# Kernel tuning notes

Hardware: AMD Instinct MI355X
Metric: run time of the kernel (lower is better)

## Reference

```python
import jax, jax.numpy as jnp
import numpy as np

# Hard-coded module constants (from source)
E = 384      # EMBEDDING_SIZE
H = 6        # HEAD_NO
HS = 64      # HEAD_SIZE = E // H
T_CTX = 256  # CONTEXT_LENGTH
L = 6        # LAYER_NO
V = 50257    # vocab_size (init kwarg)
B = 16       # batch
T = 256      # sequence length (== context length)


def setup_inputs() -> dict:
    key = jax.random.key(0)
    ks = jax.random.split(key, 12)
    p = lambda k, shape: jax.random.normal(k, shape, dtype=jnp.float32) * 0.02
    return {
        "idx": jax.random.randint(ks[0], (B, T), 0, V),
        "tok_emb": p(ks[1], (V, E)),
        "pos_emb": p(ks[2], (T_CTX, E)),
        # per-layer stacked params; per-head q/k/v weights concatenated into [E, E]
        "Wq": p(ks[3], (L, E, E)),
        "Wk": p(ks[4], (L, E, E)),
        "Wv": p(ks[5], (L, E, E)),
        "Wo": p(ks[6], (L, E, E)),
        "bo": jnp.zeros((L, E), jnp.float32),
        "ln1_g": jnp.ones((L, E), jnp.float32),
        "ln1_b": jnp.zeros((L, E), jnp.float32),
        "ln2_g": jnp.ones((L, E), jnp.float32),
        "ln2_b": jnp.zeros((L, E), jnp.float32),
        "Wm": p(ks[7], (L, E, E)),  # MLP: single Linear(E,E) + ReLU
        "bm": jnp.zeros((L, E), jnp.float32),
        "lnf_g": jnp.ones((E,), jnp.float32),
        "lnf_b": jnp.zeros((E,), jnp.float32),
        "Wlm": p(ks[8], (E, V)),
        "blm": jnp.zeros((V,), jnp.float32),
    }


def _layernorm(x, g, b):
    mu = jnp.mean(x, axis=-1, keepdims=True)
    var = jnp.var(x, axis=-1, keepdims=True)  # biased, matches torch LayerNorm
    return (x - mu) / jnp.sqrt(var + 1e-5) * g + b


def _forward(idx, tok_emb, pos_emb, Wq, Wk, Wv, Wo, bo, ln1_g, ln1_b,
             ln2_g, ln2_b, Wm, bm, lnf_g, lnf_b, Wlm, blm):
    Bb, Tt = idx.shape
    x = tok_emb[idx] + pos_emb[:Tt]                        # [B,T,E]
    causal = jnp.tril(jnp.ones((Tt, Tt), bool))            # tril buffer
    scale = 1.0 / jnp.sqrt(jnp.float32(HS))

    def block(x, lp):
        wq, wk, wv, wo, bo_, g1, b1, g2, b2, wm, bm_ = lp
        h = _layernorm(x, g1, b1)
        q = (h @ wq).reshape(Bb, Tt, H, HS)
        k = (h @ wk).reshape(Bb, Tt, H, HS)
        v = (h @ wv).reshape(Bb, Tt, H, HS)
        s = jnp.einsum('bqhd,bkhd->bhqk', q, k)
        # source: masked_fill(-inf) then divide by sqrt(HS); -inf stays -inf
        s = jnp.where(causal, s, -jnp.inf) * scale
        a = jax.nn.softmax(s, axis=-1)                     # dropout: eval mode (no-op)
        o = jnp.einsum('bhqk,bkhd->bqhd', a, v).reshape(Bb, Tt, E)
        x = x + (o @ wo + bo_)                             # proj + residual
        h2 = _layernorm(x, g2, b2)
        x = x + jax.nn.relu(h2 @ wm + bm_)                 # MLP is Linear+ReLU only
        return x, None

    x, _ = jax.lax.scan(block, x, (Wq, Wk, Wv, Wo, bo, ln1_g, ln1_b,
                                   ln2_g, ln2_b, Wm, bm))
    x = _layernorm(x, lnf_g, lnf_b)
    return x @ Wlm + blm                                   # [B,T,V] logits


def reference(idx, tok_emb, pos_emb, Wq, Wk, Wv, Wo, bo, ln1_g, ln1_b,
              ln2_g, ln2_b, Wm, bm, lnf_g, lnf_b, Wlm, blm):
    return _forward(idx, tok_emb, pos_emb, Wq, Wk, Wv, Wo, bo, ln1_g, ln1_b,
                    ln2_g, ln2_b, Wm, bm, lnf_g, lnf_b, Wlm, blm)
```

## Files before the change

kernel.cpp:

```cpp
#include <hip/hip_runtime.h>
#include <hip/hip_bf16.h>
#include <math.h>

#define E_DIM 384
#define N_HEAD 6
#define HEAD_SZ 64
#define SEQ 256
#define BATCH 16
#define NTOK 4096
#define NLAYER 6
#define VOCAB 50257
#define VPAD 50304
#define QKV_N 1152
#define NBH 96

typedef __attribute__((ext_vector_type(8))) short bf16x8;
typedef __attribute__((ext_vector_type(4))) float f32x4;

__device__ __forceinline__ void gload16(const void* g, void* l) {
    __builtin_amdgcn_global_load_lds((const __attribute__((address_space(1))) char*)g,
                                     (__attribute__((address_space(3))) char*)l, 16, 0, 0);
}

__global__ void embed_kernel(const int* __restrict__ idx,
                             const float* __restrict__ tok,
                             const float* __restrict__ pos,
                             float* __restrict__ x) {
    int i = blockIdx.x * blockDim.x + threadIdx.x;
    if (i >= NTOK * E_DIM) return;
    int m = i / E_DIM, e = i - m * E_DIM;
    int t = m & (SEQ - 1);
    x[i] = tok[(size_t)idx[m] * E_DIM + e] + pos[t * E_DIM + e];
}

__global__ __launch_bounds__(256) void ln_kernel(const float* __restrict__ x,
                                                 const float* __restrict__ g,
                                                 const float* __restrict__ b,
                                                 __hip_bfloat16* __restrict__ h) {
    int lane = threadIdx.x & 63;
    int wave = threadIdx.x >> 6;
    int row  = blockIdx.x * 4 + wave;
    const float* xr = x + (size_t)row * E_DIM;
    float v[6];
    float s = 0.f;
#pragma unroll
    for (int c = 0; c < 6; ++c) { v[c] = xr[lane + 64 * c]; s += v[c]; }
#pragma unroll
    for (int off = 32; off > 0; off >>= 1) s += __shfl_xor(s, off);
    float mu = s * (1.0f / E_DIM);
    float s2 = 0.f;
#pragma unroll
    for (int c = 0; c < 6; ++c) { float d = v[c] - mu; s2 += d * d; }
#pragma unroll
    for (int off = 32; off > 0; off >>= 1) s2 += __shfl_xor(s2, off);
    float rstd = rsqrtf(s2 * (1.0f / E_DIM) + 1e-5f);
    __hip_bfloat16* hr = h + (size_t)row * E_DIM;
#pragma unroll
    for (int c = 0; c < 6; ++c) {
        int e = lane + 64 * c;
        hr[e] = __float2bfloat16((v[c] - mu) * rstd * g[e] + b[e]);
    }
}

__device__ __forceinline__ void tconv_tile(const float* __restrict__ src,
                                           __hip_bfloat16* __restrict__ dst,
                                           int K, int N, int n0, int k0) {
    __shared__ float tbuf[64][65];
    int c = threadIdx.x & 63, r4 = threadIdx.x >> 6;
#pragma unroll
    for (int i = 0; i < 16; ++i) {
        int r = r4 * 16 + i;
        float v = 0.f;
        if (n0 + c < N) v = src[(size_t)(k0 + r) * N + n0 + c];
        tbuf[r][c] = v;
    }
    __syncthreads();
#pragma unroll
    for (int i = 0; i < 16; ++i) {
        int rn = r4 * 16 + i;
        dst[(size_t)(n0 + rn) * K + k0 + c] = __float2bfloat16(tbuf[c][rn]);
    }
}

__global__ __launch_bounds__(256) void tconv_layers(const float* __restrict__ Wq,
                                                    const float* __restrict__ Wk,
                                                    const float* __restrict__ Wv,
                                                    const float* __restrict__ Wo,
                                                    const float* __restrict__ Wm,
                                                    __hip_bfloat16* __restrict__ WtL) {
    int z = blockIdx.z;
    int l = z / 5, t = z - l * 5;
    const float* src;
    int dstoff;
    switch (t) {
        case 0: src = Wq; dstoff = 0;    break;
        case 1: src = Wk; dstoff = 384;  break;
        case 2: src = Wv; dstoff = 768;  break;
        case 3: src = Wo; dstoff = 1152; break;
        default: src = Wm; dstoff = 1536;
    }
    src += (size_t)l * E_DIM * E_DIM;
    __hip_bfloat16* dst = WtL + ((size_t)l * 1920 + dstoff) * E_DIM;
    tconv_tile(src, dst, E_DIM, E_DIM, blockIdx.x * 64, blockIdx.y * 64);
}

__global__ __launch_bounds__(256) void tconv_lm(const float* __restrict__ Wlm,
                                                __hip_bfloat16* __restrict__ dst) {
    tconv_tile(Wlm, dst, E_DIM, VOCAB, blockIdx.x * 64, blockIdx.y * 64);
}

__global__ __launch_bounds__(256) void qkvgemm(const __hip_bfloat16* __restrict__ A,
                                               const __hip_bfloat16* __restrict__ Bt,
                                               __hip_bfloat16* __restrict__ qb,
                                               __hip_bfloat16* __restrict__ kb,
                                               __hip_bfloat16* __restrict__ vt) {
    __shared__ __align__(1024) char lds[32768];
    char* Ar = lds;
    char* Br = lds + 16384;
    int tid = threadIdx.x;
    int lane = tid & 63, w = tid >> 6;
    int wm = w >> 1, wn = w & 1;
    int row0 = blockIdx.y * 128;
    int col0 = blockIdx.x * 128;

    f32x4 acc[4][4];
#pragma unroll
    for (int i = 0; i < 4; ++i)
#pragma unroll
        for (int j = 0; j < 4; ++j) acc[i][j] = (f32x4){0.f, 0.f, 0.f, 0.f};

    for (int k0 = 0; k0 < E_DIM; k0 += 64) {
        __syncthreads();
#pragma unroll
        for (int i = 0; i < 4; ++i) {
            int p  = i * 4096 + tid * 16;
            int lg = p ^ (((p >> 7) & 7) << 4);
            int r  = lg >> 7, cb = lg & 127;
            gload16((const char*)(A  + (size_t)(row0 + r) * E_DIM + k0) + cb, Ar + i * 4096 + w * 1024);
            gload16((const char*)(Bt + (size_t)(col0 + r) * E_DIM + k0) + cb, Br + i * 4096 + w * 1024);
        }
        __syncthreads();
#pragma unroll
        for (int ks = 0; ks < 2; ++ks) {
            bf16x8 af[4], bfr[4];
#pragma unroll
            for (int mi = 0; mi < 4; ++mi) {
                int rl = wm * 64 + mi * 16 + (lane & 15);
                int lg = rl * 128 + ks * 64 + ((lane >> 4) << 4);
                int ph = lg ^ ((rl & 7) << 4);
                af[mi] = *(const bf16x8*)(Ar + ph);
            }
#pragma unroll
            for (int ni = 0; ni < 4; ++ni) {
                int rl = wn * 64 + ni * 16 + (lane & 15);
                int lg = rl * 128 + ks * 64 + ((lane >> 4) << 4);
                int ph = lg ^ ((rl & 7) << 4);
                bfr[ni] = *(const bf16x8*)(Br + ph);
            }
#pragma unroll
            for (int mi = 0; mi < 4; ++mi)
#pragma unroll
                for (int ni = 0; ni < 4; ++ni)
                    acc[mi][ni] = __builtin_amdgcn_mfma_f32_16x16x32_bf16(
                        af[mi], bfr[ni], acc[mi][ni], 0, 0, 0);
        }
    }

#pragma unroll
    for (int mi = 0; mi < 4; ++mi) {
#pragma unroll
        for (int ni = 0; ni < 4; ++ni) {
            int gcl = col0 + wn * 64 + ni * 16 + (lane & 15);
            int which = gcl / 384;
            int rem = gcl - which * 384;
            int h = rem >> 6, d = rem & 63;
            int gr0 = row0 + wm * 64 + mi * 16 + ((lane >> 4) << 2);
#pragma unroll
            for (int j = 0; j < 4; ++j) {
                int gr = gr0 + j;
                int b = gr >> 8, t = gr & 255;
                int bh = b * N_HEAD + h;
                __hip_bfloat16 v = __float2bfloat16(acc[mi][ni][j]);
                if (which == 0)      qb[(((size_t)bh << 8) + t) * 64 + d] = v;
                else if (which == 1) kb[(((size_t)bh << 8) + t) * 64 + d] = v;
                else                 vt[(((size_t)bh << 6) + d) * SEQ + t] = v;
            }
        }
    }
}

template <int RELU>
__global__ __launch_bounds__(256) void egemm_ln(const __hip_bfloat16* __restrict__ A,
                                                const __hip_bfloat16* __restrict__ Bt,
                                                const float* __restrict__ bias,
                                                const float* __restrict__ xin,
                                                float* __restrict__ xout,
                                                const float* __restrict__ g,
                                                const float* __restrict__ bvec,
                                                __hip_bfloat16* __restrict__ hout) {
    __shared__ __align__(1024) char lds[53248];
    char* Breg = lds;
    char* Areg = lds + 49152;
    float* xt = (float*)lds;
    int tid = threadIdx.x;
    int lane = tid & 63, w = tid >> 6;
    int row0 = blockIdx.x * 32;

    f32x4 acc[2][6];
#pragma unroll
    for (int i = 0; i < 2; ++i)
#pragma unroll
        for (int j = 0; j < 6; ++j) acc[i][j] = (f32x4){0.f, 0.f, 0.f, 0.f};

    for (int k0 = 0; k0 < E_DIM; k0 += 64) {
        __syncthreads();
        {
            int p  = tid * 16;
            int lg = p ^ (((p >> 7) & 7) << 4);
            int r  = lg >> 7, cb = lg & 127;
            gload16((const char*)(A + (size_t)(row0 + r) * E_DIM + k0) + cb, Areg + w * 1024);
        }
#pragma unroll
        for (int i = 0; i < 12; ++i) {
            int p  = i * 4096 + tid * 16;
            int lg = p ^ (((p >> 7) & 7) << 4);
            int r  = lg >> 7, cb = lg & 127;
            gload16((const char*)(Bt + (size_t)r * E_DIM + k0) + cb, Breg + i * 4096 + w * 1024);
        }
        __syncthreads();
#pragma unroll
        for (int ks = 0; ks < 2; ++ks) {
            bf16x8 af[2], bfr[6];
#pragma unroll
            for (int mi = 0; mi < 2; ++mi) {
                int rl = mi * 16 + (lane & 15);
                int lg = rl * 128 + ks * 64 + ((lane >> 4) << 4);
                int ph = lg ^ ((rl & 7) << 4);
                af[mi] = *(const bf16x8*)(Areg + ph);
            }
#pragma unroll
            for (int ni = 0; ni < 6; ++ni) {
                int rl = w * 96 + ni * 16 + (lane & 15);
                int lg = rl * 128 + ks * 64 + ((lane >> 4) << 4);
                int ph = lg ^ ((rl & 7) << 4);
                bfr[ni] = *(const bf16x8*)(Breg + ph);
            }
#pragma unroll
            for (int mi = 0; mi < 2; ++mi)
#pragma unroll
                for (int ni = 0; ni < 6; ++ni)
                    acc[mi][ni] = __builtin_amdgcn_mfma_f32_16x16x32_bf16(
                        af[mi], bfr[ni], acc[mi][ni], 0, 0, 0);
        }
    }
    __syncthreads();

#pragma unroll
    for (int mi = 0; mi < 2; ++mi) {
#pragma unroll
        for (int ni = 0; ni < 6; ++ni) {
            int gc = w * 96 + ni * 16 + (lane & 15);
            int lr0 = mi * 16 + ((lane >> 4) << 2);
            float bv = bias[gc];
#pragma unroll
            for (int j = 0; j < 4; ++j) {
                int lr = lr0 + j;
                float u = acc[mi][ni][j] + bv;
                if (RELU) u = fmaxf(u, 0.f);
                float xn = xin[(size_t)(row0 + lr) * E_DIM + gc] + u;
                xout[(size_t)(row0 + lr) * E_DIM + gc] = xn;
                xt[lr * 392 + gc] = xn;
            }
        }
    }
    __syncthreads();

#pragma unroll
    for (int r8 = 0; r8 < 8; ++r8) {
        int r = w * 8 + r8;
        float v[6];
        float s = 0.f;
#pragma unroll
        for (int c = 0; c < 6; ++c) { v[c] = xt[r * 392 + lane + 64 * c]; s += v[c]; }
#pragma unroll
        for (int off = 32; off > 0; off >>= 1) s += __shfl_xor(s, off);
        float mu = s * (1.0f / E_DIM);
        float s2 = 0.f;
#pragma unroll
        for (int c = 0; c < 6; ++c) { float d = v[c] - mu; s2 += d * d; }
#pragma unroll
        for (int off = 32; off > 0; off >>= 1) s2 += __shfl_xor(s2, off);
        float rstd = rsqrtf(s2 * (1.0f / E_DIM) + 1e-5f);
        __hip_bfloat16* hr = hout + (size_t)(row0 + r) * E_DIM;
#pragma unroll
        for (int c = 0; c < 6; ++c) {
            int e = lane + 64 * c;
            hr[e] = __float2bfloat16((v[c] - mu) * rstd * g[e] + bvec[e]);
        }
    }
}

__global__ __launch_bounds__(256) void mgemm_lm(const __hip_bfloat16* __restrict__ A,
                                                const __hip_bfloat16* __restrict__ Bt,
                                                const float* __restrict__ bias,
                                                float* __restrict__ C) {
    __shared__ __align__(1024) char lds[32768];
    char* Ar = lds;
    char* Br = lds + 16384;
    int tid = threadIdx.x;
    int lane = tid & 63, w = tid >> 6;
    int wm = w >> 1, wn = w & 1;
    int row0 = blockIdx.y * 128;
    int col0 = blockIdx.x * 128;

    f32x4 acc[4][4];
#pragma unroll
    for (int i = 0; i < 4; ++i)
#pragma unroll
        for (int j = 0; j < 4; ++j) acc[i][j] = (f32x4){0.f, 0.f, 0.f, 0.f};

    for (int k0 = 0; k0 < E_DIM; k0 += 64) {
        __syncthreads();
#pragma unroll
        for (int i = 0; i < 4; ++i) {
            int p  = i * 4096 + tid * 16;
            int lg = p ^ (((p >> 7) & 7) << 4);
            int r  = lg >> 7, cb = lg & 127;
            gload16((const char*)(A  + (size_t)(row0 + r) * E_DIM + k0) + cb, Ar + i * 4096 + w * 1024);
            gload16((const char*)(Bt + (size_t)(col0 + r) * E_DIM + k0) + cb, Br + i * 4096 + w * 1024);
        }
        __syncthreads();
#pragma unroll
        for (int ks = 0; ks < 2; ++ks) {
            bf16x8 af[4], bfr[4];
#pragma unroll
            for (int mi = 0; mi < 4; ++mi) {
                int rl = wm * 64 + mi * 16 + (lane & 15);
                int lg = rl * 128 + ks * 64 + ((lane >> 4) << 4);
                int ph = lg ^ ((rl & 7) << 4);
                af[mi] = *(const bf16x8*)(Ar + ph);
            }
#pragma unroll
            for (int ni = 0; ni < 4; ++ni) {
                int rl = wn * 64 + ni * 16 + (lane & 15);
                int lg = rl * 128 + ks * 64 + ((lane >> 4) << 4);
                int ph = lg ^ ((rl & 7) << 4);
                bfr[ni] = *(const bf16x8*)(Br + ph);
            }
#pragma unroll
            for (int mi = 0; mi < 4; ++mi)
#pragma unroll
                for (int ni = 0; ni < 4; ++ni)
                    acc[mi][ni] = __builtin_amdgcn_mfma_f32_16x16x32_bf16(
                        af[mi], bfr[ni], acc[mi][ni], 0, 0, 0);
        }
    }

#pragma unroll
    for (int mi = 0; mi < 4; ++mi) {
#pragma unroll
        for (int ni = 0; ni < 4; ++ni) {
            int gr = row0 + wm * 64 + mi * 16 + ((lane >> 4) << 2);
            int gc = col0 + wn * 64 + ni * 16 + (lane & 15);
            if (gc < VOCAB) {
                float bv = bias[gc];
#pragma unroll
                for (int j = 0; j < 4; ++j)
                    C[(size_t)(gr + j) * VOCAB + gc] = acc[mi][ni][j] + bv;
            }
        }
    }
}

#define ATT_K 0
#define ATT_V 32768
#define ATT_Q 65536

__global__ __launch_bounds__(256) void attn_fused(const __hip_bfloat16* __restrict__ qb,
                                                  const __hip_bfloat16* __restrict__ kb,
                                                  const __hip_bfloat16* __restrict__ vt,
                                                  __hip_bfloat16* __restrict__ o) {
    __shared__ __align__(1024) char lds[73728];
    int tid = threadIdx.x;
    int lane = tid & 63, w = tid >> 6;
    int bh = blockIdx.x;
    int mq = blockIdx.y;
    int b = bh / N_HEAD, h = bh - b * N_HEAD;

    const char* kg = (const char*)(kb + (size_t)bh * SEQ * 64);
#pragma unroll
    for (int i = 0; i < 8; ++i) {
        int p = i * 4096 + tid * 16;
        int lg = p ^ (((p >> 7) & 7) << 4);
        gload16(kg + lg, lds + ATT_K + p);
    }
    const char* vg = (const char*)(vt + (size_t)bh * 64 * SEQ);
#pragma unroll
    for (int i = 0; i < 8; ++i) {
        int p = i * 4096 + tid * 16;
        int lg = p ^ (((p >> 9) & 7) << 4);
        gload16(vg + lg, lds + ATT_V + p);
    }
    const char* qg = (const char*)(qb + ((size_t)bh * SEQ + mq * 64) * 64);
#pragma unroll
    for (int i = 0; i < 2; ++i) {
        int p = i * 4096 + tid * 16;
        int lg = p ^ (((p >> 7) & 7) << 4);
        gload16(qg + lg, lds + ATT_Q + p);
    }
    __syncthreads();

    int q0 = w * 16;
    int qg0 = mq * 64 + q0;

    f32x4 acc[16];
#pragma unroll
    for (int n = 0; n < 16; ++n) acc[n] = (f32x4){0.f, 0.f, 0.f, 0.f};
#pragma unroll
    for (int ks = 0; ks < 2; ++ks) {
        int rq = q0 + (lane & 15);
        int byq = (ks * 64 + ((lane >> 4) << 4)) ^ ((rq & 7) << 4);
        bf16x8 aq = *(const bf16x8*)(lds + ATT_Q + rq * 128 + byq);
#pragma unroll
        for (int n = 0; n < 16; ++n) {
            int rk = n * 16 + (lane & 15);
            int byk = (ks * 64 + ((lane >> 4) << 4)) ^ ((rk & 7) << 4);
            bf16x8 bk = *(const bf16x8*)(lds + ATT_K + rk * 128 + byk);
            acc[n] = __builtin_amdgcn_mfma_f32_16x16x32_bf16(aq, bk, acc[n], 0, 0, 0);
        }
    }
    __syncthreads();

    char* pbase = lds + ATT_K + w * 8192;
#pragma unroll
    for (int j = 0; j < 4; ++j) {
        int rql = ((lane >> 4) << 2) + j;
        int rg = qg0 + rql;
        float s[16];
        float m = -INFINITY;
#pragma unroll
        for (int n = 0; n < 16; ++n) {
            int cg = n * 16 + (lane & 15);
            float v = (cg <= rg) ? acc[n][j] * 0.125f : -INFINITY;
            s[n] = v;
            m = fmaxf(m, v);
        }
#pragma unroll
        for (int off = 1; off < 16; off <<= 1) m = fmaxf(m, __shfl_xor(m, off));
        float sum = 0.f;
#pragma unroll
        for (int n = 0; n < 16; ++n) { s[n] = __expf(s[n] - m); sum += s[n]; }
#pragma unroll
        for (int off = 1; off < 16; off <<= 1) sum += __shfl_xor(sum, off);
        float inv = 1.0f / sum;
#pragma unroll
        for (int n = 0; n < 16; ++n) {
            int cg = n * 16 + (lane & 15);
            int by = (cg * 2) ^ ((rql & 7) << 4);
            *(__hip_bfloat16*)(pbase + rql * 512 + by) = __float2bfloat16(s[n] * inv);
        }
    }

    f32x4 oacc[4];
#pragma unroll
    for (int nf = 0; nf < 4; ++nf) oacc[nf] = (f32x4){0.f, 0.f, 0.f, 0.f};
#pragma unroll
    for (int ks = 0; ks < 8; ++ks) {
        int rp = lane & 15;
        int byp = (ks * 64 + ((lane >> 4) << 4)) ^ ((rp & 7) << 4);
        bf16x8 ap = *(const bf16x8*)(pbase + rp * 512 + byp);
#pragma unroll
        for (int nf = 0; nf < 4; ++nf) {
            int rv = nf * 16 + (lane & 15);
            int byv = (ks * 64 + ((lane >> 4) << 4)) ^ ((rv & 7) << 4);
            bf16x8 bv = *(const bf16x8*)(lds + ATT_V + rv * 512 + byv);
            oacc[nf] = __builtin_amdgcn_mfma_f32_16x16x32_bf16(ap, bv, oacc[nf], 0, 0, 0);
        }
    }

#pragma unroll
    for (int nf = 0; nf < 4; ++nf) {
#pragma unroll
        for (int j = 0; j < 4; ++j) {
            int t = mq * 64 + q0 + ((lane >> 4) << 2) + j;
            int d = nf * 16 + (lane & 15);
            o[(size_t)(b * SEQ + t) * E_DIM + h * 64 + d] = __float2bfloat16(oacc[nf][j]);
        }
    }
}

extern "C" void kernel_launch(void* const* d_in, const int* in_sizes, int n_in,
                              void* d_out, int out_size, void* d_ws, size_t ws_size,
                              hipStream_t stream) {
    const int*   idx  = (const int*)d_in[0];
    const float* tok  = (const float*)d_in[1];
    const float* pos  = (const float*)d_in[2];
    const float* Wq   = (const float*)d_in[3];
    const float* Wk   = (const float*)d_in[4];
    const float* Wv   = (const float*)d_in[5];
    const float* Wo   = (const float*)d_in[6];
    const float* bo   = (const float*)d_in[7];
    const float* ln1g = (const float*)d_in[8];
    const float* ln1b = (const float*)d_in[9];
    const float* ln2g = (const float*)d_in[10];
    const float* ln2b = (const float*)d_in[11];
    const float* Wm   = (const float*)d_in[12];
    const float* bm   = (const float*)d_in[13];
    const float* lnfg = (const float*)d_in[14];
    const float* lnfb = (const float*)d_in[15];
    const float* Wlm  = (const float*)d_in[16];
    const float* blm  = (const float*)d_in[17];
    float* out = (float*)d_out;

    float*           x    = (float*)d_ws;
    __hip_bfloat16*  hb   = (__hip_bfloat16*)(x + (size_t)NTOK * E_DIM);
    __hip_bfloat16*  WtL  = hb + (size_t)NTOK * E_DIM;
    __hip_bfloat16*  WtLM = WtL + (size_t)NLAYER * 1920 * E_DIM;
    __hip_bfloat16*  qbv  = WtLM + (size_t)VPAD * E_DIM;
    __hip_bfloat16*  kbv  = qbv + (size_t)NBH * SEQ * 64;
    __hip_bfloat16*  vtb  = kbv + (size_t)NBH * SEQ * 64;

    embed_kernel<<<(NTOK * E_DIM + 255) / 256, 256, 0, stream>>>(idx, tok, pos, x);
    tconv_layers<<<dim3(6, 6, NLAYER * 5), 256, 0, stream>>>(Wq, Wk, Wv, Wo, Wm, WtL);
    tconv_lm<<<dim3(VPAD / 64, E_DIM / 64), 256, 0, stream>>>(Wlm, WtLM);
    ln_kernel<<<NTOK / 4, 256, 0, stream>>>(x, ln1g, ln1b, hb);

    for (int l = 0; l < NLAYER; ++l) {
        const __hip_bfloat16* wl = WtL + (size_t)l * 1920 * E_DIM;
        qkvgemm<<<dim3(QKV_N / 128, NTOK / 128), 256, 0, stream>>>(hb, wl, qbv, kbv, vtb);
        attn_fused<<<dim3(NBH, 4), 256, 0, stream>>>(qbv, kbv, vtb, hb);
        egemm_ln<0><<<NTOK / 32, 256, 0, stream>>>(hb, wl + (size_t)1152 * E_DIM,
                                                   bo + l * E_DIM, x, x,
                                                   ln2g + l * E_DIM, ln2b + l * E_DIM, hb);
        const float* ng = (l == NLAYER - 1) ? lnfg : ln1g + (l + 1) * E_DIM;
        const float* nb = (l == NLAYER - 1) ? lnfb : ln1b + (l + 1) * E_DIM;
        egemm_ln<1><<<NTOK / 32, 256, 0, stream>>>(hb, wl + (size_t)1536 * E_DIM,
                                                   bm + l * E_DIM, x, x,
                                                   ng, nb, hb);
    }

    mgemm_lm<<<dim3(VPAD / 128, NTOK / 128), 256, 0, stream>>>(hb, WtLM, blm, out);
}
```

Baseline: 866.5 us.

## Double-buffer LDS tiles in QKV and residual GEMMs, swizzle LM-head block order

The QKV GEMM and the fused residual/LayerNorm GEMM now keep two LDS buffers. Global-to-LDS loads for the next K tile are issued before the MFMA work on the current tile, so load latency overlaps compute instead of being serialized. The LM-head GEMM remaps its flat block index with a stride of 8, which groups blocks that likely share tiles onto the same XCD and L2. The cost is doubled LDS per block (about 104 KB in the residual GEMM), which cuts how many blocks can be resident per CU.

After: 754.7 us. -12.9%, faster.

```diff
diff --git a/kernel.cpp b/kernel.cpp
--- a/kernel.cpp
+++ b/kernel.cpp
@@ -114,9 +114,7 @@
                                                __hip_bfloat16* __restrict__ qb,
                                                __hip_bfloat16* __restrict__ kb,
                                                __hip_bfloat16* __restrict__ vt) {
-    __shared__ __align__(1024) char lds[32768];
-    char* Ar = lds;
-    char* Br = lds + 16384;
+    __shared__ __align__(1024) char lds[65536];
     int tid = threadIdx.x;
     int lane = tid & 63, w = tid >> 6;
     int wm = w >> 1, wn = w & 1;
@@ -129,17 +127,25 @@
 #pragma unroll
         for (int j = 0; j < 4; ++j) acc[i][j] = (f32x4){0.f, 0.f, 0.f, 0.f};
 
-    for (int k0 = 0; k0 < E_DIM; k0 += 64) {
-        __syncthreads();
+    auto stage = [&](int buf, int k0) {
+        char* Ab = lds + buf * 32768;
+        char* Bb = Ab + 16384;
 #pragma unroll
         for (int i = 0; i < 4; ++i) {
             int p  = i * 4096 + tid * 16;
             int lg = p ^ (((p >> 7) & 7) << 4);
             int r  = lg >> 7, cb = lg & 127;
-            gload16((const char*)(A  + (size_t)(row0 + r) * E_DIM + k0) + cb, Ar + i * 4096 + w * 1024);
-            gload16((const char*)(Bt + (size_t)(col0 + r) * E_DIM + k0) + cb, Br + i * 4096 + w * 1024);
-        }
+            gload16((const char*)(A  + (size_t)(row0 + r) * E_DIM + k0) + cb, Ab + i * 4096 + w * 1024);
+            gload16((const char*)(Bt + (size_t)(col0 + r) * E_DIM + k0) + cb, Bb + i * 4096 + w * 1024);
+        }
+    };
+
+    stage(0, 0);
+    for (int kt = 0; kt < 6; ++kt) {
         __syncthreads();
+        if (kt < 5) stage((kt + 1) & 1, (kt + 1) * 64);
+        const char* Ab = lds + (kt & 1) * 32768;
+        const char* Bb = Ab + 16384;
 #pragma unroll
         for (int ks = 0; ks < 2; ++ks) {
             bf16x8 af[4], bfr[4];
@@ -148,14 +154,14 @@
                 int rl = wm * 64 + mi * 16 + (lane & 15);
                 int lg = rl * 128 + ks * 64 + ((lane >> 4) << 4);
                 int ph = lg ^ ((rl & 7) << 4);
-                af[mi] = *(const bf16x8*)(Ar + ph);
+                af[mi] = *(const bf16x8*)(Ab + ph);
             }
 #pragma unroll
             for (int ni = 0; ni < 4; ++ni) {
                 int rl = wn * 64 + ni * 16 + (lane & 15);
                 int lg = rl * 128 + ks * 64 + ((lane >> 4) << 4);
                 int ph = lg ^ ((rl & 7) << 4);
-                bfr[ni] = *(const bf16x8*)(Br + ph);
+                bfr[ni] = *(const bf16x8*)(Bb + ph);
             }
 #pragma unroll
             for (int mi = 0; mi < 4; ++mi)
@@ -198,9 +204,7 @@
                                                 const float* __restrict__ g,
                                                 const float* __restrict__ bvec,
                                                 __hip_bfloat16* __restrict__ hout) {
-    __shared__ __align__(1024) char lds[53248];
-    char* Breg = lds;
-    char* Areg = lds + 49152;
+    __shared__ __align__(1024) char lds[106496];
     float* xt = (float*)lds;
     int tid = threadIdx.x;
     int lane = tid & 63, w = tid >> 6;
@@ -212,22 +216,30 @@
 #pragma unroll
         for (int j = 0; j < 6; ++j) acc[i][j] = (f32x4){0.f, 0.f, 0.f, 0.f};
 
-    for (int k0 = 0; k0 < E_DIM; k0 += 64) {
-        __syncthreads();
+    auto stage = [&](int buf, int k0) {
+        char* Bb = lds + buf * 53248;
+        char* Ab = Bb + 49152;
         {
             int p  = tid * 16;
             int lg = p ^ (((p >> 7) & 7) << 4);
             int r  = lg >> 7, cb = lg & 127;
-            gload16((const char*)(A + (size_t)(row0 + r) * E_DIM + k0) + cb, Areg + w * 1024);
+            gload16((const char*)(A + (size_t)(row0 + r) * E_DIM + k0) + cb, Ab + w * 1024);
         }
 #pragma unroll
         for (int i = 0; i < 12; ++i) {
             int p  = i * 4096 + tid * 16;
             int lg = p ^ (((p >> 7) & 7) << 4);
             int r  = lg >> 7, cb = lg & 127;
-            gload16((const char*)(Bt + (size_t)r * E_DIM + k0) + cb, Breg + i * 4096 + w * 1024);
-        }
+            gload16((const char*)(Bt + (size_t)r * E_DIM + k0) + cb, Bb + i * 4096 + w * 1024);
+        }
+    };
+
+    stage(0, 0);
+    for (int kt = 0; kt < 6; ++kt) {
         __syncthreads();
+        if (kt < 5) stage((kt + 1) & 1, (kt + 1) * 64);
+        const char* Bb = lds + (kt & 1) * 53248;
+        const char* Ab = Bb + 49152;
 #pragma unroll
         for (int ks = 0; ks < 2; ++ks) {
             bf16x8 af[2], bfr[6];
@@ -236,14 +248,14 @@
                 int rl = mi * 16 + (lane & 15);
                 int lg = rl * 128 + ks * 64 + ((lane >> 4) << 4);
                 int ph = lg ^ ((rl & 7) << 4);
-                af[mi] = *(const bf16x8*)(Areg + ph);
+                af[mi] = *(const bf16x8*)(Ab + ph);
             }
 #pragma unroll
             for (int ni = 0; ni < 6; ++ni) {
                 int rl = w * 96 + ni * 16 + (lane & 15);
                 int lg = rl * 128 + ks * 64 + ((lane >> 4) << 4);
                 int ph = lg ^ ((rl & 7) << 4);
-                bfr[ni] = *(const bf16x8*)(Breg + ph);
+                bfr[ni] = *(const bf16x8*)(Bb + ph);
             }
 #pragma unroll
             for (int mi = 0; mi < 2; ++mi)
@@ -310,8 +322,12 @@
     int tid = threadIdx.x;
     int lane = tid & 63, w = tid >> 6;
     int wm = w >> 1, wn = w & 1;
-    int row0 = blockIdx.y * 128;
-    int col0 = blockIdx.x * 128;
+
+    int wg  = blockIdx.y * 393 + blockIdx.x;
+    int swz = (wg & 7) * 1572 + (wg >> 3);
+    int bx  = swz % 393, by = swz / 393;
+    int row0 = by * 128;
+    int col0 = bx * 128;
 
     f32x4 acc[4][4];
 #pragma unroll
```
